# Optimization experiments

Hardware: AMD Instinct MI355X
Metric: run time of the kernel (lower is better)

## Reference

```python
import jax, jax.numpy as jnp
import numpy as np

H = 1024      # LSTM_DIM
D = 1024      # BERT_DIM
VW = 30000    # word vocab
VA = 30       # action vocab
T = 64        # transition steps
S = 512       # BERT memory length


def lstm_cell(x, h, c, Wih, Whh, bih, bhh):
    # torch.nn.LSTMCell math: gates ordered i, f, g, o
    g = x @ Wih.T + bih + h @ Whh.T + bhh
    i, f, gg, o = jnp.split(g, 4, axis=-1)
    c2 = jax.nn.sigmoid(f) * c + jax.nn.sigmoid(i) * jnp.tanh(gg)
    h2 = jax.nn.sigmoid(o) * jnp.tanh(c2)
    return h2, c2


def forward(memory, actions, words,
            term_Wih, term_Whh, term_bih, term_bhh,
            act_Wih, act_Whh, act_bih, act_bhh,
            Wq, bq, Wa1, ba1, Wa2, ba2, Ww1, bw1, Ww2, bw2,
            act_emb, word_emb):
    z = jnp.zeros((1, H), dtype=memory.dtype)

    def step(carry, xs):
        term_h, term_c, act_h, act_c, stack_h = carry
        a_t, w_t = xs
        # predict_action: concat decoder states, dot-attention over BERT memory (no softmax)
        states = jnp.concatenate([term_h, act_h, stack_h], axis=1)     # [1, 3H]
        q = states @ Wq.T + bq                                          # [1, D]
        attn = jnp.einsum('bsd,bd->bs', memory, q)                      # [1, S]
        ctx = jnp.einsum('bs,bsd->bd', attn, memory)                    # [1, D]
        final = jnp.concatenate([states, ctx], axis=1)                  # [1, 3H+D]
        act_logits = jax.nn.relu(final @ Wa1.T + ba1) @ Wa2.T + ba2     # [1, VA]
        word_logits = jax.nn.relu(final @ Ww1.T + bw1) @ Ww2.T + bw2    # [1, VW]
        # do_action: act LSTM step, then SHIFT: word embedding into term LSTM + stack push
        a_e = act_emb[a_t][None, :]
        act_h2, act_c2 = lstm_cell(a_e, act_h, act_c, act_Wih, act_Whh, act_bih, act_bhh)
        w_e = word_emb[w_t][None, :]
        term_h2, term_c2 = lstm_cell(w_e, term_h, term_c, term_Wih, term_Whh, term_bih, term_bhh)
        new_carry = (term_h2, term_c2, act_h2, act_c2, w_e)
        return new_carry, (act_logits[0], word_logits[0])

    carry0 = (z, z, z, z, z)
    _, (act_logits, word_logits) = jax.lax.scan(step, carry0, (actions, words))
    return act_logits, word_logits  # [T, VA], [T, VW]


def setup_inputs() -> dict:
    key = jax.random.key(0)
    ks = jax.random.split(key, 24)
    s = 0.02

    def n(k, shape):
        return jax.random.normal(k, shape, dtype=jnp.float32) * s

    return {
        'memory': jax.random.normal(ks[0], (1, S, D), dtype=jnp.float32),
        'actions': jax.random.randint(ks[1], (T,), 0, VA),
        'words': jax.random.randint(ks[2], (T,), 0, VW),
        'term_Wih': n(ks[3], (4 * H, H)), 'term_Whh': n(ks[4], (4 * H, H)),
        'term_bih': n(ks[5], (4 * H,)), 'term_bhh': n(ks[6], (4 * H,)),
        'act_Wih': n(ks[7], (4 * H, H)), 'act_Whh': n(ks[8], (4 * H, H)),
        'act_bih': n(ks[9], (4 * H,)), 'act_bhh': n(ks[10], (4 * H,)),
        'Wq': n(ks[11], (D, 3 * H)), 'bq': n(ks[12], (D,)),
        'Wa1': n(ks[13], (H, 3 * H + D)), 'ba1': n(ks[14], (H,)),
        'Wa2': n(ks[15], (VA, H)), 'ba2': n(ks[16], (VA,)),
        'Ww1': n(ks[17], (H, 3 * H + D)), 'bw1': n(ks[18], (H,)),
        'Ww2': n(ks[19], (VW, H)), 'bw2': n(ks[20], (VW,)),
        'act_emb': n(ks[21], (VA, H)),
        'word_emb': n(ks[22], (VW, H)),
    }


def reference(memory, actions, words,
              term_Wih, term_Whh, term_bih, term_bhh,
              act_Wih, act_Whh, act_bih, act_bhh,
              Wq, bq, Wa1, ba1, Wa2, ba2, Ww1, bw1, Ww2, bw2,
              act_emb, word_emb):
    return forward(memory, actions, words,
                   term_Wih, term_Whh, term_bih, term_bhh,
                   act_Wih, act_Whh, act_bih, act_bhh,
                   Wq, bq, Wa1, ba1, Wa2, ba2, Ww1, bw1, Ww2, bw2,
                   act_emb, word_emb)
```

## Files before the change

kernel.cpp:

```cpp
#include <hip/hip_runtime.h>

#define H 1024
#define T_STEPS 64
#define S_MEM 512
#define VA 30
#define VW 30000

typedef unsigned long long u64;
typedef __attribute__((ext_vector_type(8))) short short8;
typedef __attribute__((ext_vector_type(4))) float f32x4;

__device__ __forceinline__ float sigmf(float x) { return 1.f / (1.f + expf(-x)); }
__device__ __forceinline__ unsigned short f2bf(float f) {
  unsigned u = __float_as_uint(f);
  return (unsigned short)((u + 0x7FFFu + ((u >> 16) & 1u)) >> 16);
}
__device__ __forceinline__ short8 ldcvt8(const float* p) {
  float4 f0 = *(const float4*)p;
  float4 f1 = *(const float4*)(p + 4);
  short8 r;
  r[0] = (short)f2bf(f0.x); r[1] = (short)f2bf(f0.y);
  r[2] = (short)f2bf(f0.z); r[3] = (short)f2bf(f0.w);
  r[4] = (short)f2bf(f1.x); r[5] = (short)f2bf(f1.y);
  r[6] = (short)f2bf(f1.z); r[7] = (short)f2bf(f1.w);
  return r;
}
__device__ __forceinline__ void stage_sw(float* S, int nn, int km, float4 v) {
  int c2 = ((nn >> 2) ^ km) & 15, p = nn & 3;
  S[(km * 4 + 0) * 64 + c2 * 4 + p] = v.x;
  S[(km * 4 + 1) * 64 + c2 * 4 + p] = v.y;
  S[(km * 4 + 2) * 64 + c2 * 4 + p] = v.z;
  S[(km * 4 + 3) * 64 + c2 * 4 + p] = v.w;
}
__device__ __forceinline__ void mm_inner(const float* As, const float* Bs,
                                         int ridx, int cidx, float (&acc)[4][4]) {
  const float4* As4 = (const float4*)As;
  const float4* Bs4 = (const float4*)Bs;
  __syncthreads();
#pragma unroll 8
  for (int kk = 0; kk < 64; ++kk) {
    int sw = kk >> 2;
    float4 a4 = As4[kk * 16 + ((ridx ^ sw) & 15)];
    float4 b4 = Bs4[kk * 16 + ((cidx ^ sw) & 15)];
    float av[4] = {a4.x, a4.y, a4.z, a4.w};
    float bv[4] = {b4.x, b4.y, b4.z, b4.w};
#pragma unroll
    for (int i = 0; i < 4; ++i)
#pragma unroll
      for (int j = 0; j < 4; ++j) acc[i][j] += av[i] * bv[j];
  }
  __syncthreads();
}

__global__ __launch_bounds__(256) void k_head(
    const int* __restrict__ actions, const int* __restrict__ words,
    const float* __restrict__ act_emb, const float* __restrict__ word_emb,
    const float* __restrict__ Wih_t, const float* __restrict__ Wih_a,
    float* __restrict__ Pxg_t, float* __restrict__ Pxg_a,
    float* __restrict__ fin, u64* __restrict__ htag) {
  int x = blockIdx.x, tid = threadIdx.x, y = blockIdx.y, z = blockIdx.z;
  if (x == 64) {
    int bi = y * 2 + z;
    uint4* hq = (uint4*)(htag) + (size_t)bi * 16384;
    uint4 zz = make_uint4(0, 0, 0, 0);
    for (int i = tid; i < 16384; i += 256) hq[i] = zz;
    if (bi == 0)
      for (int i = tid; i < 3072; i += 256) fin[i] = 0.f;
    if (bi == 1) {
      for (int j = tid; j < 63 * 1024; j += 256) {
        int t = j >> 10, i2 = j & 1023;
        fin[(size_t)(t + 1) * 4096 + 2048 + i2] = word_emb[(size_t)words[t] * 1024 + i2];
      }
    }
    return;
  }
  __shared__ __align__(16) float As[4096], Bs[4096];
  const int* idxs = z ? actions : words;
  const float* emb = z ? act_emb : word_emb;
  const float* B = z ? Wih_a : Wih_t;
  float* Pp = z ? Pxg_a : Pxg_t;
  int cidx = tid & 15, ridx = tid >> 4;
  int n0 = x * 64, kbeg = y * 512;
  float acc[4][4] = {};
  for (int k0 = kbeg; k0 < kbeg + 512; k0 += 64) {
#pragma unroll
    for (int i = 0; i < 4; ++i) {
      int f = tid + i * 256, rr = f >> 4, km = f & 15;
      float4 v = *(const float4*)&emb[(size_t)idxs[rr] * 1024 + k0 + km * 4];
      stage_sw(As, rr, km, v);
    }
#pragma unroll
    for (int i = 0; i < 4; ++i) {
      int f = tid + i * 256, nn = f >> 4, km = f & 15;
      float4 v = *(const float4*)&B[(size_t)(n0 + nn) * 1024 + k0 + km * 4];
      stage_sw(Bs, nn, km, v);
    }
    mm_inner(As, Bs, ridx, cidx, acc);
  }
  int gcol = n0 + cidx * 4;
  float* P = Pp + (size_t)y * 262144;
#pragma unroll
  for (int i = 0; i < 4; ++i) {
    int row = ridx * 4 + i;
    *(float4*)&P[(size_t)row * 4096 + gcol] =
        make_float4(acc[i][0], acc[i][1], acc[i][2], acc[i][3]);
  }
}

__global__ __launch_bounds__(256, 1) void k_recur(
    const float* __restrict__ Whh_term, const float* __restrict__ Whh_act,
    const float* __restrict__ Pxg_term, const float* __restrict__ Pxg_act,
    const float* __restrict__ bih_t, const float* __restrict__ bhh_t,
    const float* __restrict__ bih_a, const float* __restrict__ bhh_a,
    float* __restrict__ fin, u64* __restrict__ htag) {
  __shared__ float hs[2][32 * 36];
  __shared__ float xgs[63 * 32];
  int b = blockIdx.x, tid = threadIdx.x;
  int lstm = b >> 7, k0 = (b & 127) * 8;
  const float* Whh = lstm ? Whh_act : Whh_term;
  const float* Pxg = lstm ? Pxg_act : Pxg_term;
  const float* bih = lstm ? bih_a : bih_t;
  const float* bhh = lstm ? bhh_a : bhh_t;
  int d = tid >> 5, p = tid & 31;

  float wreg[128];
#pragma unroll
  for (int g = 0; g < 4; ++g) {
    const float* wrow = Whh + (size_t)(g * 1024 + k0 + d) * 1024 + p * 32;
#pragma unroll
    for (int i = 0; i < 32; i += 4) {
      float4 v = *(const float4*)(wrow + i);
      wreg[g * 32 + i]     = v.x; wreg[g * 32 + i + 1] = v.y;
      wreg[g * 32 + i + 2] = v.z; wreg[g * 32 + i + 3] = v.w;
    }
  }
#pragma unroll
  for (int i = 0; i < 128; ++i) asm volatile("" : "+v"(wreg[i]));

  for (int i = tid; i < 63 * 32; i += 256) {
    int rr = i & 31, t2 = i >> 5;
    int row2 = (rr >> 3) * 1024 + k0 + (rr & 7);
    xgs[i] = Pxg[(size_t)t2 * 4096 + row2] + Pxg[262144 + (size_t)t2 * 4096 + row2] +
             bih[row2] + bhh[row2];
  }
  float c_loc = 0.f;

  for (int t = 0; t < 63; ++t) {
    float* hb = hs[t & 1];
    if (t > 0) {
      const u64* src = htag + (size_t)t * 2048 + lstm * 1024;
      u64 v0 = __hip_atomic_load(&src[tid], __ATOMIC_RELAXED, __HIP_MEMORY_SCOPE_AGENT);
      u64 v1 = __hip_atomic_load(&src[tid + 256], __ATOMIC_RELAXED, __HIP_MEMORY_SCOPE_AGENT);
      u64 v2 = __hip_atomic_load(&src[tid + 512], __ATOMIC_RELAXED, __HIP_MEMORY_SCOPE_AGENT);
      u64 v3 = __hip_atomic_load(&src[tid + 768], __ATOMIC_RELAXED, __HIP_MEMORY_SCOPE_AGENT);
      while ((unsigned)(v0 >> 32) != (unsigned)t) {
        __builtin_amdgcn_s_sleep(1);
        v0 = __hip_atomic_load(&src[tid], __ATOMIC_RELAXED, __HIP_MEMORY_SCOPE_AGENT);
      }
      while ((unsigned)(v1 >> 32) != (unsigned)t) {
        __builtin_amdgcn_s_sleep(1);
        v1 = __hip_atomic_load(&src[tid + 256], __ATOMIC_RELAXED, __HIP_MEMORY_SCOPE_AGENT);
      }
      while ((unsigned)(v2 >> 32) != (unsigned)t) {
        __builtin_amdgcn_s_sleep(1);
        v2 = __hip_atomic_load(&src[tid + 512], __ATOMIC_RELAXED, __HIP_MEMORY_SCOPE_AGENT);
      }
      while ((unsigned)(v3 >> 32) != (unsigned)t) {
        __builtin_amdgcn_s_sleep(1);
        v3 = __hip_atomic_load(&src[tid + 768], __ATOMIC_RELAXED, __HIP_MEMORY_SCOPE_AGENT);
      }
      hb[((tid) >> 5) * 36 + (tid & 31)]       = __uint_as_float((unsigned)v0);
      hb[((tid + 256) >> 5) * 36 + (tid & 31)] = __uint_as_float((unsigned)v1);
      hb[((tid + 512) >> 5) * 36 + (tid & 31)] = __uint_as_float((unsigned)v2);
      hb[((tid + 768) >> 5) * 36 + (tid & 31)] = __uint_as_float((unsigned)v3);
    } else {
#pragma unroll
      for (int j = 0; j < 4; ++j) {
        int idx = tid + j * 256;
        hb[(idx >> 5) * 36 + (idx & 31)] = 0.f;
      }
    }
    __syncthreads();

    const float* hp = hb + p * 36;
    float s0 = 0.f, s1 = 0.f, s2 = 0.f, s3 = 0.f;
#pragma unroll
    for (int i = 0; i < 32; i += 4) {
      float4 hv = *(const float4*)&hp[i];
      s0 += wreg[i] * hv.x + wreg[i + 1] * hv.y + wreg[i + 2] * hv.z + wreg[i + 3] * hv.w;
      s1 += wreg[32 + i] * hv.x + wreg[33 + i] * hv.y + wreg[34 + i] * hv.z + wreg[35 + i] * hv.w;
      s2 += wreg[64 + i] * hv.x + wreg[65 + i] * hv.y + wreg[66 + i] * hv.z + wreg[67 + i] * hv.w;
      s3 += wreg[96 + i] * hv.x + wreg[97 + i] * hv.y + wreg[98 + i] * hv.z + wreg[99 + i] * hv.w;
    }
#pragma unroll
    for (int m = 1; m <= 16; m <<= 1) {
      s0 += __shfl_xor(s0, m); s1 += __shfl_xor(s1, m);
      s2 += __shfl_xor(s2, m); s3 += __shfl_xor(s3, m);
    }
    if (p == 0) {
      float gi = s0 + xgs[t * 32 + d];
      float gf = s1 + xgs[t * 32 + 8 + d];
      float gg = s2 + xgs[t * 32 + 16 + d];
      float go = s3 + xgs[t * 32 + 24 + d];
      float c2 = sigmf(gf) * c_loc + sigmf(gi) * tanhf(gg);
      float h2 = sigmf(go) * tanhf(c2);
      c_loc = c2;
      fin[(size_t)(t + 1) * 4096 + lstm * 1024 + k0 + d] = h2;
      __hip_atomic_store(&htag[(size_t)(t + 1) * 2048 + lstm * 1024 + k0 + d],
                         (((u64)(t + 1)) << 32) | (u64)__float_as_uint(h2),
                         __ATOMIC_RELAXED, __HIP_MEMORY_SCOPE_AGENT);
    }
  }
}

__global__ __launch_bounds__(256) void k_mfma_bt(
    const float* __restrict__ A, int lda,
    const float* __restrict__ B0, const float* __restrict__ B1, int ldb,
    const float* __restrict__ bias0, const float* __restrict__ bias1,
    float* __restrict__ out0, float* __restrict__ out1, int ldc,
    int K, int relu) {
  __shared__ __align__(16) float sm[4 * 1024];
  const float* B = blockIdx.y ? B1 : B0;
  const float* bias = blockIdx.y ? bias1 : bias0;
  float* out = blockIdx.y ? out1 : out0;
  int tid = threadIdx.x;
  int w = tid >> 6, lane = tid & 63;
  int col0 = blockIdx.x * 16;
  int klen = K >> 2;
  int kbeg = w * klen;
  int kg = kbeg + (lane >> 4) * 8;
  const float* brow = B + (size_t)(col0 + (lane & 15)) * ldb + kg;
  const float* arow = A + (size_t)(lane & 15) * lda + kg;
  f32x4 acc0 = {0.f, 0.f, 0.f, 0.f}, acc1 = acc0, acc2 = acc0, acc3 = acc0;

  short8 bf = ldcvt8(brow);
  short8 a0 = ldcvt8(arow);
  short8 a1 = ldcvt8(arow + 16 * lda);
  short8 a2 = ldcvt8(arow + 32 * lda);
  short8 a3 = ldcvt8(arow + 48 * lda);
  for (int k0 = 0; k0 < klen - 32; k0 += 32) {
    short8 bf_n = ldcvt8(brow + k0 + 32);
    short8 a0n = ldcvt8(arow + k0 + 32);
    short8 a1n = ldcvt8(arow + 16 * lda + k0 + 32);
    short8 a2n = ldcvt8(arow + 32 * lda + k0 + 32);
    short8 a3n = ldcvt8(arow + 48 * lda + k0 + 32);
    acc0 = __builtin_amdgcn_mfma_f32_16x16x32_bf16(a0, bf, acc0, 0, 0, 0);
    acc1 = __builtin_amdgcn_mfma_f32_16x16x32_bf16(a1, bf, acc1, 0, 0, 0);
    acc2 = __builtin_amdgcn_mfma_f32_16x16x32_bf16(a2, bf, acc2, 0, 0, 0);
    acc3 = __builtin_amdgcn_mfma_f32_16x16x32_bf16(a3, bf, acc3, 0, 0, 0);
    bf = bf_n; a0 = a0n; a1 = a1n; a2 = a2n; a3 = a3n;
  }
  acc0 = __builtin_amdgcn_mfma_f32_16x16x32_bf16(a0, bf, acc0, 0, 0, 0);
  acc1 = __builtin_amdgcn_mfma_f32_16x16x32_bf16(a1, bf, acc1, 0, 0, 0);
  acc2 = __builtin_amdgcn_mfma_f32_16x16x32_bf16(a2, bf, acc2, 0, 0, 0);
  acc3 = __builtin_amdgcn_mfma_f32_16x16x32_bf16(a3, bf, acc3, 0, 0, 0);

  {
    int rbase = (lane >> 4) * 4, c = lane & 15;
    float* smw = sm + w * 1024;
#pragma unroll
    for (int j = 0; j < 4; ++j) {
      smw[(rbase + j) * 16 + c]      = acc0[j];
      smw[(16 + rbase + j) * 16 + c] = acc1[j];
      smw[(32 + rbase + j) * 16 + c] = acc2[j];
      smw[(48 + rbase + j) * 16 + c] = acc3[j];
    }
  }
  __syncthreads();
  {
    const float4* sm4 = (const float4*)sm;
    float4 v = sm4[tid];
    float4 v1 = sm4[256 + tid], v2 = sm4[512 + tid], v3 = sm4[768 + tid];
    v.x += v1.x + v2.x + v3.x;
    v.y += v1.y + v2.y + v3.y;
    v.z += v1.z + v2.z + v3.z;
    v.w += v1.w + v2.w + v3.w;
    int e0 = tid * 4;
    int row = e0 >> 4, cofs = e0 & 15;
    float4 b = *(const float4*)&bias[col0 + cofs];
    v.x += b.x; v.y += b.y; v.z += b.z; v.w += b.w;
    if (relu) {
      v.x = fmaxf(v.x, 0.f); v.y = fmaxf(v.y, 0.f);
      v.z = fmaxf(v.z, 0.f); v.w = fmaxf(v.w, 0.f);
    }
    *(float4*)&out[(size_t)row * ldc + col0 + cofs] = v;
  }
}

__global__ __launch_bounds__(256) void k_attn2(
    const float* __restrict__ qbuf, const float* __restrict__ mem,
    float* __restrict__ Pa) {
  __shared__ __align__(16) float As[4096], Bs[4096];
  int tid = threadIdx.x, cidx = tid & 15, ridx = tid >> 4;
  int n0 = blockIdx.x * 64, kbeg = blockIdx.y * 128;
  float acc[4][4] = {};
  for (int k0 = kbeg; k0 < kbeg + 128; k0 += 64) {
#pragma unroll
    for (int i = 0; i < 4; ++i) {
      int f = tid + i * 256, rr = f >> 4, km = f & 15;
      float4 v = *(const float4*)&qbuf[(size_t)rr * 1024 + k0 + km * 4];
      stage_sw(As, rr, km, v);
    }
#pragma unroll
    for (int i = 0; i < 4; ++i) {
      int f = tid + i * 256, nn = f >> 4, km = f & 15;
      float4 v = *(const float4*)&mem[(size_t)(n0 + nn) * 1024 + k0 + km * 4];
      stage_sw(Bs, nn, km, v);
    }
    mm_inner(As, Bs, ridx, cidx, acc);
  }
  int gcol = n0 + cidx * 4;
  float* P = Pa + (size_t)blockIdx.y * 32768;
#pragma unroll
  for (int i = 0; i < 4; ++i) {
    int row = ridx * 4 + i;
    *(float4*)&P[(size_t)row * 512 + gcol] =
        make_float4(acc[i][0], acc[i][1], acc[i][2], acc[i][3]);
  }
}

__global__ __launch_bounds__(256) void k_ctx2(
    const float* __restrict__ Pa, const float* __restrict__ mem,
    float* __restrict__ fin) {
  __shared__ __align__(16) float As[4096], Bs[4096];
  int tid = threadIdx.x, cidx = tid & 15, ridx = tid >> 4;
  int n0 = blockIdx.x * 64;
  float acc[4][4] = {};
  for (int k0 = 0; k0 < 512; k0 += 64) {
#pragma unroll
    for (int i = 0; i < 4; ++i) {
      int f = tid + i * 256, rr = f >> 4, km = f & 15;
      int col = k0 + km * 4;
      float4 v = make_float4(0.f, 0.f, 0.f, 0.f);
#pragma unroll
      for (int s = 0; s < 8; ++s) {
        float4 p = *(const float4*)&Pa[(size_t)s * 32768 + (size_t)rr * 512 + col];
        v.x += p.x; v.y += p.y; v.z += p.z; v.w += p.w;
      }
      stage_sw(As, rr, km, v);
    }
#pragma unroll
    for (int i = 0; i < 4; ++i) {
      int f = tid + i * 256, kr = f >> 4, nq = f & 15;
      float4 v = *(const float4*)&mem[(size_t)(k0 + kr) * 1024 + n0 + nq * 4];
      ((float4*)Bs)[kr * 16 + ((nq ^ (kr >> 2)) & 15)] = v;
    }
    mm_inner(As, Bs, ridx, cidx, acc);
  }
  int gcol = n0 + cidx * 4;
#pragma unroll
  for (int i = 0; i < 4; ++i) {
    int row = ridx * 4 + i;
    *(float4*)&fin[(size_t)row * 4096 + 3072 + gcol] =
        make_float4(acc[i][0], acc[i][1], acc[i][2], acc[i][3]);
  }
}

__global__ __launch_bounds__(256) void k_actlog(
    const float* __restrict__ ha, const float* __restrict__ Wa2,
    const float* __restrict__ ba2, float* __restrict__ out) {
  int t = blockIdx.x, tid = threadIdx.x;
  int v = tid >> 3, p = tid & 7;
  float sum = 0.f;
  if (v < VA) {
    const float* a  = ha + (size_t)t * 1024 + p * 128;
    const float* wr = Wa2 + (size_t)v * 1024 + p * 128;
#pragma unroll 8
    for (int i = 0; i < 128; i += 4) {
      float4 av = *(const float4*)(a + i);
      float4 wv = *(const float4*)(wr + i);
      sum += av.x * wv.x + av.y * wv.y + av.z * wv.z + av.w * wv.w;
    }
  }
  sum += __shfl_xor(sum, 1);
  sum += __shfl_xor(sum, 2);
  sum += __shfl_xor(sum, 4);
  if (p == 0 && v < VA) out[(size_t)t * VA + v] = sum + ba2[v];
}

extern "C" void kernel_launch(void* const* d_in, const int* in_sizes, int n_in,
                              void* d_out, int out_size, void* d_ws, size_t ws_size,
                              hipStream_t stream) {
  const float* memory   = (const float*)d_in[0];
  const int*   actions  = (const int*)d_in[1];
  const int*   words    = (const int*)d_in[2];
  const float* term_Wih = (const float*)d_in[3];
  const float* term_Whh = (const float*)d_in[4];
  const float* term_bih = (const float*)d_in[5];
  const float* term_bhh = (const float*)d_in[6];
  const float* act_Wih  = (const float*)d_in[7];
  const float* act_Whh  = (const float*)d_in[8];
  const float* act_bih  = (const float*)d_in[9];
  const float* act_bhh  = (const float*)d_in[10];
  const float* Wq  = (const float*)d_in[11];
  const float* bq  = (const float*)d_in[12];
  const float* Wa1 = (const float*)d_in[13];
  const float* ba1 = (const float*)d_in[14];
  const float* Wa2 = (const float*)d_in[15];
  const float* ba2 = (const float*)d_in[16];
  const float* Ww1 = (const float*)d_in[17];
  const float* bw1 = (const float*)d_in[18];
  const float* Ww2 = (const float*)d_in[19];
  const float* bw2 = (const float*)d_in[20];
  const float* act_emb  = (const float*)d_in[21];
  const float* word_emb = (const float*)d_in[22];
  float* out = (float*)d_out;

  float* w     = (float*)d_ws;
  float* fin   = w;
  u64*   htag  = (u64*)(w + 262144);
  float* Pxg_t = w + 525312;
  float* Pxg_a = w + 1049600;
  float* qbuf  = w + 525312;
  float* Pa    = w + 590848;
  float* ha    = w + 852992;
  float* hw    = w + 918528;

  k_head<<<dim3(65, 2, 2), 256, 0, stream>>>(
      actions, words, act_emb, word_emb, term_Wih, act_Wih,
      Pxg_t, Pxg_a, fin, htag);

  k_recur<<<256, 256, 0, stream>>>(term_Whh, act_Whh, Pxg_t, Pxg_a,
                                   term_bih, term_bhh, act_bih, act_bhh, fin, htag);

  k_mfma_bt<<<dim3(64, 1), 256, 0, stream>>>(
      fin, 4096, Wq, nullptr, 3072, bq, nullptr, qbuf, nullptr, 1024, 3072, 0);

  k_attn2<<<dim3(8, 8), 256, 0, stream>>>(qbuf, memory, Pa);

  k_ctx2<<<16, 256, 0, stream>>>(Pa, memory, fin);

  k_mfma_bt<<<dim3(64, 2), 256, 0, stream>>>(
      fin, 4096, Wa1, Ww1, 4096, ba1, bw1, ha, hw, 1024, 4096, 1);

  k_actlog<<<64, 256, 0, stream>>>(ha, Wa2, ba2, out);

  k_mfma_bt<<<dim3(1875, 1), 256, 0, stream>>>(
      hw, 1024, Ww2, nullptr, 1024, bw2, nullptr, out + 1920, nullptr, VW, 1024, 0);
}
```

Before: 474.6 us.

## Precompute memory Gram matrix folded into Wq, overlapped with LSTM recurrence

Because attention has no softmax, ctx equals q·(MᵀM), so the change precomputes M2=MᵀM, a transformed query weight WpT=M2·Wq and bias bq2=M2·bq. These are computed inside the recurrence kernel by extra blocks that run alongside the LSTM blocks, coordinated through an atomic counter. The separate q, attention and ctx kernels become a single split-K GEMM whose partial sums are reduced inside the Wa1/Ww1 GEMM, and the final reduction writes bf16 hw for a new word-logit MFMA kernel. The cost is the extra weight-sized work and a spin-wait in the recurrence kernel, which may compete with the latency-critical LSTM blocks. The reassociated summation order also changes floating-point rounding.

```diff
diff --git a/kernel.cpp b/kernel.cpp
--- a/kernel.cpp
+++ b/kernel.cpp
@@ -51,13 +51,25 @@
   }
   __syncthreads();
 }
+__device__ __forceinline__ void st4a(float* p, float4 v) {
+  u64 lo = ((u64)__float_as_uint(v.y) << 32) | __float_as_uint(v.x);
+  u64 hi = ((u64)__float_as_uint(v.w) << 32) | __float_as_uint(v.z);
+  __hip_atomic_store((u64*)p, lo, __ATOMIC_RELAXED, __HIP_MEMORY_SCOPE_AGENT);
+  __hip_atomic_store(((u64*)p) + 1, hi, __ATOMIC_RELAXED, __HIP_MEMORY_SCOPE_AGENT);
+}
+__device__ __forceinline__ float4 ld4a(const float* p) {
+  u64 lo = __hip_atomic_load((const u64*)p, __ATOMIC_RELAXED, __HIP_MEMORY_SCOPE_AGENT);
+  u64 hi = __hip_atomic_load(((const u64*)p) + 1, __ATOMIC_RELAXED, __HIP_MEMORY_SCOPE_AGENT);
+  return make_float4(__uint_as_float((unsigned)lo), __uint_as_float((unsigned)(lo >> 32)),
+                     __uint_as_float((unsigned)hi), __uint_as_float((unsigned)(hi >> 32)));
+}
 
 __global__ __launch_bounds__(256) void k_head(
     const int* __restrict__ actions, const int* __restrict__ words,
     const float* __restrict__ act_emb, const float* __restrict__ word_emb,
     const float* __restrict__ Wih_t, const float* __restrict__ Wih_a,
     float* __restrict__ Pxg_t, float* __restrict__ Pxg_a,
-    float* __restrict__ fin, u64* __restrict__ htag) {
+    float* __restrict__ fin, u64* __restrict__ htag, int* __restrict__ m2ctr) {
   int x = blockIdx.x, tid = threadIdx.x, y = blockIdx.y, z = blockIdx.z;
   if (x == 64) {
     int bi = y * 2 + z;
@@ -72,6 +84,7 @@
         fin[(size_t)(t + 1) * 4096 + 2048 + i2] = word_emb[(size_t)words[t] * 1024 + i2];
       }
     }
+    if (bi == 2 && tid < 8) m2ctr[tid] = 0;
     return;
   }
   __shared__ __align__(16) float As[4096], Bs[4096];
@@ -112,10 +125,93 @@
     const float* __restrict__ Pxg_term, const float* __restrict__ Pxg_act,
     const float* __restrict__ bih_t, const float* __restrict__ bhh_t,
     const float* __restrict__ bih_a, const float* __restrict__ bhh_a,
-    float* __restrict__ fin, u64* __restrict__ htag) {
+    float* __restrict__ fin, u64* __restrict__ htag,
+    const float* __restrict__ memory, const float* __restrict__ Wq,
+    const float* __restrict__ bq, float* __restrict__ M2,
+    float* __restrict__ WpT, float* __restrict__ bq2, int* __restrict__ m2ctr) {
   __shared__ float hs[2][32 * 36];
   __shared__ float xgs[63 * 32];
+  __shared__ __align__(16) float As[4096], Bs[4096];
   int b = blockIdx.x, tid = threadIdx.x;
+  int cidx = tid & 15, ridx = tid >> 4;
+
+  if (b >= 256) {
+    if (b < 512) {
+      int idx = b - 256;
+      int i0 = (idx >> 4) * 64, j0 = (idx & 15) * 64;
+      float acc[4][4] = {};
+      for (int k0 = 0; k0 < 512; k0 += 64) {
+#pragma unroll
+        for (int i = 0; i < 4; ++i) {
+          int f = tid + i * 256, kr = f >> 4, nq = f & 15;
+          float4 v = *(const float4*)&memory[(size_t)(k0 + kr) * 1024 + i0 + nq * 4];
+          ((float4*)As)[kr * 16 + ((nq ^ (kr >> 2)) & 15)] = v;
+        }
+#pragma unroll
+        for (int i = 0; i < 4; ++i) {
+          int f = tid + i * 256, kr = f >> 4, nq = f & 15;
+          float4 v = *(const float4*)&memory[(size_t)(k0 + kr) * 1024 + j0 + nq * 4];
+          ((float4*)Bs)[kr * 16 + ((nq ^ (kr >> 2)) & 15)] = v;
+        }
+        mm_inner(As, Bs, ridx, cidx, acc);
+      }
+      int gcol = j0 + cidx * 4;
+#pragma unroll
+      for (int i = 0; i < 4; ++i)
+        st4a(&M2[(size_t)(i0 + ridx * 4 + i) * 1024 + gcol],
+             make_float4(acc[i][0], acc[i][1], acc[i][2], acc[i][3]));
+      asm volatile("s_waitcnt vmcnt(0)" ::: "memory");
+      __syncthreads();
+      if (tid == 0)
+        __hip_atomic_fetch_add(&m2ctr[0], 1, __ATOMIC_RELAXED, __HIP_MEMORY_SCOPE_AGENT);
+      return;
+    }
+    if (tid == 0) {
+      while (__hip_atomic_load(&m2ctr[0], __ATOMIC_RELAXED, __HIP_MEMORY_SCOPE_AGENT) < 256)
+        __builtin_amdgcn_s_sleep(8);
+    }
+    __syncthreads();
+    if (b == 704) {
+      for (int n = tid; n < 1024; n += 256) {
+        float s = 0.f;
+        for (int d = 0; d < 1024; d += 4) {
+          float4 m = ld4a(&M2[(size_t)n * 1024 + d]);
+          float4 bv = *(const float4*)&bq[d];
+          s += m.x * bv.x + m.y * bv.y + m.z * bv.z + m.w * bv.w;
+        }
+        bq2[n] = s;
+      }
+      return;
+    }
+    int idx = b - 512;
+    for (int q = 0; q < 4; ++q) {
+      int t = idx * 4 + q;
+      int n0 = (t / 48) * 64, m0 = (t % 48) * 64;
+      float acc[4][4] = {};
+      for (int k0 = 0; k0 < 1024; k0 += 64) {
+#pragma unroll
+        for (int i = 0; i < 4; ++i) {
+          int f = tid + i * 256, rr = f >> 4, km = f & 15;
+          float4 v = ld4a(&M2[(size_t)(n0 + rr) * 1024 + k0 + km * 4]);
+          stage_sw(As, rr, km, v);
+        }
+#pragma unroll
+        for (int i = 0; i < 4; ++i) {
+          int f = tid + i * 256, kr = f >> 4, nq = f & 15;
+          float4 v = *(const float4*)&Wq[(size_t)(k0 + kr) * 3072 + m0 + nq * 4];
+          ((float4*)Bs)[kr * 16 + ((nq ^ (kr >> 2)) & 15)] = v;
+        }
+        mm_inner(As, Bs, ridx, cidx, acc);
+      }
+      int gcol = m0 + cidx * 4;
+#pragma unroll
+      for (int i = 0; i < 4; ++i)
+        *(float4*)&WpT[(size_t)(n0 + ridx * 4 + i) * 3072 + gcol] =
+            make_float4(acc[i][0], acc[i][1], acc[i][2], acc[i][3]);
+    }
+    return;
+  }
+
   int lstm = b >> 7, k0 = (b & 127) * 8;
   const float* Whh = lstm ? Whh_act : Whh_term;
   const float* Pxg = lstm ? Pxg_act : Pxg_term;
@@ -213,146 +309,118 @@
   }
 }
 
-__global__ __launch_bounds__(256) void k_mfma_bt(
+__global__ __launch_bounds__(256) void k_gemm64(
     const float* __restrict__ A, int lda,
-    const float* __restrict__ B0, const float* __restrict__ B1, int ldb,
-    const float* __restrict__ bias0, const float* __restrict__ bias1,
-    float* __restrict__ out0, float* __restrict__ out1, int ldc,
-    int K, int relu) {
-  __shared__ __align__(16) float sm[4 * 1024];
-  const float* B = blockIdx.y ? B1 : B0;
-  const float* bias = blockIdx.y ? bias1 : bias0;
-  float* out = blockIdx.y ? out1 : out0;
-  int tid = threadIdx.x;
-  int w = tid >> 6, lane = tid & 63;
-  int col0 = blockIdx.x * 16;
-  int klen = K >> 2;
-  int kbeg = w * klen;
-  int kg = kbeg + (lane >> 4) * 8;
-  const float* brow = B + (size_t)(col0 + (lane & 15)) * ldb + kg;
-  const float* arow = A + (size_t)(lane & 15) * lda + kg;
-  f32x4 acc0 = {0.f, 0.f, 0.f, 0.f}, acc1 = acc0, acc2 = acc0, acc3 = acc0;
-
-  short8 bf = ldcvt8(brow);
-  short8 a0 = ldcvt8(arow);
-  short8 a1 = ldcvt8(arow + 16 * lda);
-  short8 a2 = ldcvt8(arow + 32 * lda);
-  short8 a3 = ldcvt8(arow + 48 * lda);
-  for (int k0 = 0; k0 < klen - 32; k0 += 32) {
-    short8 bf_n = ldcvt8(brow + k0 + 32);
-    short8 a0n = ldcvt8(arow + k0 + 32);
-    short8 a1n = ldcvt8(arow + 16 * lda + k0 + 32);
-    short8 a2n = ldcvt8(arow + 32 * lda + k0 + 32);
-    short8 a3n = ldcvt8(arow + 48 * lda + k0 + 32);
-    acc0 = __builtin_amdgcn_mfma_f32_16x16x32_bf16(a0, bf, acc0, 0, 0, 0);
-    acc1 = __builtin_amdgcn_mfma_f32_16x16x32_bf16(a1, bf, acc1, 0, 0, 0);
-    acc2 = __builtin_amdgcn_mfma_f32_16x16x32_bf16(a2, bf, acc2, 0, 0, 0);
-    acc3 = __builtin_amdgcn_mfma_f32_16x16x32_bf16(a3, bf, acc3, 0, 0, 0);
-    bf = bf_n; a0 = a0n; a1 = a1n; a2 = a2n; a3 = a3n;
-  }
-  acc0 = __builtin_amdgcn_mfma_f32_16x16x32_bf16(a0, bf, acc0, 0, 0, 0);
-  acc1 = __builtin_amdgcn_mfma_f32_16x16x32_bf16(a1, bf, acc1, 0, 0, 0);
-  acc2 = __builtin_amdgcn_mfma_f32_16x16x32_bf16(a2, bf, acc2, 0, 0, 0);
-  acc3 = __builtin_amdgcn_mfma_f32_16x16x32_bf16(a3, bf, acc3, 0, 0, 0);
-
-  {
-    int rbase = (lane >> 4) * 4, c = lane & 15;
-    float* smw = sm + w * 1024;
-#pragma unroll
-    for (int j = 0; j < 4; ++j) {
-      smw[(rbase + j) * 16 + c]      = acc0[j];
-      smw[(16 + rbase + j) * 16 + c] = acc1[j];
-      smw[(32 + rbase + j) * 16 + c] = acc2[j];
-      smw[(48 + rbase + j) * 16 + c] = acc3[j];
-    }
-  }
-  __syncthreads();
-  {
-    const float4* sm4 = (const float4*)sm;
-    float4 v = sm4[tid];
-    float4 v1 = sm4[256 + tid], v2 = sm4[512 + tid], v3 = sm4[768 + tid];
-    v.x += v1.x + v2.x + v3.x;
-    v.y += v1.y + v2.y + v3.y;
-    v.z += v1.z + v2.z + v3.z;
-    v.w += v1.w + v2.w + v3.w;
-    int e0 = tid * 4;
-    int row = e0 >> 4, cofs = e0 & 15;
-    float4 b = *(const float4*)&bias[col0 + cofs];
-    v.x += b.x; v.y += b.y; v.z += b.z; v.w += b.w;
-    if (relu) {
-      v.x = fmaxf(v.x, 0.f); v.y = fmaxf(v.y, 0.f);
-      v.z = fmaxf(v.z, 0.f); v.w = fmaxf(v.w, 0.f);
-    }
-    *(float4*)&out[(size_t)row * ldc + col0 + cofs] = v;
-  }
-}
-
-__global__ __launch_bounds__(256) void k_attn2(
-    const float* __restrict__ qbuf, const float* __restrict__ mem,
-    float* __restrict__ Pa) {
-  __shared__ __align__(16) float As[4096], Bs[4096];
-  int tid = threadIdx.x, cidx = tid & 15, ridx = tid >> 4;
-  int n0 = blockIdx.x * 64, kbeg = blockIdx.y * 128;
-  float acc[4][4] = {};
-  for (int k0 = kbeg; k0 < kbeg + 128; k0 += 64) {
-#pragma unroll
-    for (int i = 0; i < 4; ++i) {
-      int f = tid + i * 256, rr = f >> 4, km = f & 15;
-      float4 v = *(const float4*)&qbuf[(size_t)rr * 1024 + k0 + km * 4];
-      stage_sw(As, rr, km, v);
-    }
-#pragma unroll
-    for (int i = 0; i < 4; ++i) {
-      int f = tid + i * 256, nn = f >> 4, km = f & 15;
-      float4 v = *(const float4*)&mem[(size_t)(n0 + nn) * 1024 + k0 + km * 4];
-      stage_sw(Bs, nn, km, v);
-    }
-    mm_inner(As, Bs, ridx, cidx, acc);
-  }
-  int gcol = n0 + cidx * 4;
-  float* P = Pa + (size_t)blockIdx.y * 32768;
-#pragma unroll
-  for (int i = 0; i < 4; ++i) {
-    int row = ridx * 4 + i;
-    *(float4*)&P[(size_t)row * 512 + gcol] =
-        make_float4(acc[i][0], acc[i][1], acc[i][2], acc[i][3]);
-  }
-}
-
-__global__ __launch_bounds__(256) void k_ctx2(
-    const float* __restrict__ Pa, const float* __restrict__ mem,
-    float* __restrict__ fin) {
+    const float* __restrict__ B, int ldb,
+    int N, int K, float* __restrict__ Ppart) {
   __shared__ __align__(16) float As[4096], Bs[4096];
   int tid = threadIdx.x, cidx = tid & 15, ridx = tid >> 4;
   int n0 = blockIdx.x * 64;
+  int klen = K / gridDim.y, kbeg = blockIdx.y * klen;
   float acc[4][4] = {};
-  for (int k0 = 0; k0 < 512; k0 += 64) {
+  for (int k0 = kbeg; k0 < kbeg + klen; k0 += 64) {
 #pragma unroll
     for (int i = 0; i < 4; ++i) {
       int f = tid + i * 256, rr = f >> 4, km = f & 15;
-      int col = k0 + km * 4;
-      float4 v = make_float4(0.f, 0.f, 0.f, 0.f);
-#pragma unroll
-      for (int s = 0; s < 8; ++s) {
-        float4 p = *(const float4*)&Pa[(size_t)s * 32768 + (size_t)rr * 512 + col];
-        v.x += p.x; v.y += p.y; v.z += p.z; v.w += p.w;
-      }
+      float4 v = *(const float4*)&A[(size_t)rr * lda + k0 + km * 4];
       stage_sw(As, rr, km, v);
     }
 #pragma unroll
     for (int i = 0; i < 4; ++i) {
-      int f = tid + i * 256, kr = f >> 4, nq = f & 15;
-      float4 v = *(const float4*)&mem[(size_t)(k0 + kr) * 1024 + n0 + nq * 4];
-      ((float4*)Bs)[kr * 16 + ((nq ^ (kr >> 2)) & 15)] = v;
+      int f = tid + i * 256, nn = f >> 4, km = f & 15;
+      float4 v = *(const float4*)&B[(size_t)(n0 + nn) * ldb + k0 + km * 4];
+      stage_sw(Bs, nn, km, v);
     }
     mm_inner(As, Bs, ridx, cidx, acc);
   }
   int gcol = n0 + cidx * 4;
+  float* P = Ppart + (size_t)blockIdx.y * 64 * N;
 #pragma unroll
   for (int i = 0; i < 4; ++i) {
     int row = ridx * 4 + i;
-    *(float4*)&fin[(size_t)row * 4096 + 3072 + gcol] =
+    *(float4*)&P[(size_t)row * N + gcol] =
         make_float4(acc[i][0], acc[i][1], acc[i][2], acc[i][3]);
+  }
+}
+
+__global__ __launch_bounds__(256) void k_gemm_dual(
+    const float* __restrict__ A0, int lda,
+    const float* __restrict__ B0, const float* __restrict__ B1, int ldb,
+    int N, int K, float* __restrict__ P0, float* __restrict__ P1,
+    const float* __restrict__ Pc2, const float* __restrict__ bq2, int kb) {
+  __shared__ __align__(16) float As[4096], Bs[4096];
+  const float* B = blockIdx.z ? B1 : B0;
+  float* Pp = blockIdx.z ? P1 : P0;
+  int tid = threadIdx.x, cidx = tid & 15, ridx = tid >> 4;
+  int n0 = blockIdx.x * 64;
+  int klen = K / gridDim.y, kbeg = blockIdx.y * klen;
+  float acc[4][4] = {};
+  for (int k0 = kbeg; k0 < kbeg + klen; k0 += 64) {
+#pragma unroll
+    for (int i = 0; i < 4; ++i) {
+      int f = tid + i * 256, rr = f >> 4, km = f & 15;
+      float4 v;
+      if (k0 >= kb) {
+        int kc = k0 - kb + km * 4;
+        float4 bb = *(const float4*)&bq2[kc];
+        v = bb;
+#pragma unroll
+        for (int s = 0; s < 8; ++s) {
+          float4 pp = *(const float4*)&Pc2[(size_t)s * 65536 + (size_t)rr * 1024 + kc];
+          v.x += pp.x; v.y += pp.y; v.z += pp.z; v.w += pp.w;
+        }
+      } else {
+        v = *(const float4*)&A0[(size_t)rr * lda + k0 + km * 4];
+      }
+      stage_sw(As, rr, km, v);
+    }
+#pragma unroll
+    for (int i = 0; i < 4; ++i) {
+      int f = tid + i * 256, nn = f >> 4, km = f & 15;
+      float4 v = *(const float4*)&B[(size_t)(n0 + nn) * ldb + k0 + km * 4];
+      stage_sw(Bs, nn, km, v);
+    }
+    mm_inner(As, Bs, ridx, cidx, acc);
+  }
+  int gcol = n0 + cidx * 4;
+  float* P = Pp + (size_t)blockIdx.y * 64 * N;
+#pragma unroll
+  for (int i = 0; i < 4; ++i) {
+    int row = ridx * 4 + i;
+    *(float4*)&P[(size_t)row * N + gcol] =
+        make_float4(acc[i][0], acc[i][1], acc[i][2], acc[i][3]);
+  }
+}
+
+__global__ __launch_bounds__(256) void k_reduce_dual(
+    const float* __restrict__ P0, const float* __restrict__ P1, int S, int N,
+    const float* __restrict__ ba0, const float* __restrict__ ba1,
+    float* __restrict__ o0, float* __restrict__ o1, int relu,
+    unsigned short* __restrict__ hwb_out) {
+  const float* P = blockIdx.y ? P1 : P0;
+  const float* bias = blockIdx.y ? ba1 : ba0;
+  float* out = blockIdx.y ? o1 : o0;
+  int q = blockIdx.x * 256 + threadIdx.x;
+  int total = 64 * N / 4;
+  if (q >= total) return;
+  int e0 = q * 4;
+  int col = e0 % N;
+  float4 v = make_float4(0, 0, 0, 0);
+  for (int s = 0; s < S; ++s) {
+    float4 p = *(const float4*)&P[(size_t)s * 64 * N + e0];
+    v.x += p.x; v.y += p.y; v.z += p.z; v.w += p.w;
+  }
+  float4 b = *(const float4*)&bias[col];
+  v.x += b.x; v.y += b.y; v.z += b.z; v.w += b.w;
+  if (relu) {
+    v.x = fmaxf(v.x, 0.f); v.y = fmaxf(v.y, 0.f);
+    v.z = fmaxf(v.z, 0.f); v.w = fmaxf(v.w, 0.f);
+  }
+  *(float4*)&out[e0] = v;
+  if (blockIdx.y == 1 && hwb_out) {
+    unsigned pk0 = (unsigned)f2bf(v.x) | ((unsigned)f2bf(v.y) << 16);
+    unsigned pk1 = (unsigned)f2bf(v.z) | ((unsigned)f2bf(v.w) << 16);
+    *(uint2*)&hwb_out[e0] = make_uint2(pk0, pk1);
   }
 }
 
@@ -376,6 +444,53 @@
   sum += __shfl_xor(sum, 2);
   sum += __shfl_xor(sum, 4);
   if (p == 0 && v < VA) out[(size_t)t * VA + v] = sum + ba2[v];
+}
+
+__global__ __launch_bounds__(256) void k_word_mfma(
+    const unsigned short* __restrict__ hwb, const float* __restrict__ Ww2,
+    const float* __restrict__ bw2, float* __restrict__ outw) {
+  int tid = threadIdx.x;
+  int wv = tid >> 6, lane = tid & 63;
+  int col = blockIdx.x * 64 + wv * 16 + (lane & 15);
+  int colr = col < VW ? col : VW - 1;
+  int kg = (lane >> 4) * 8;
+  const float* brow = Ww2 + (size_t)colr * 1024 + kg;
+  const unsigned short* arow = hwb + (size_t)(lane & 15) * 1024 + kg;
+  f32x4 acc0 = {0.f, 0.f, 0.f, 0.f}, acc1 = acc0, acc2 = acc0, acc3 = acc0;
+
+  short8 bf = ldcvt8(brow);
+  short8 a0 = *(const short8*)(arow);
+  short8 a1 = *(const short8*)(arow + 16 * 1024);
+  short8 a2 = *(const short8*)(arow + 32 * 1024);
+  short8 a3 = *(const short8*)(arow + 48 * 1024);
+  for (int k0 = 0; k0 < 992; k0 += 32) {
+    short8 bf_n = ldcvt8(brow + k0 + 32);
+    short8 a0n = *(const short8*)(arow + k0 + 32);
+    short8 a1n = *(const short8*)(arow + 16 * 1024 + k0 + 32);
+    short8 a2n = *(const short8*)(arow + 32 * 1024 + k0 + 32);
+    short8 a3n = *(const short8*)(arow + 48 * 1024 + k0 + 32);
+    acc0 = __builtin_amdgcn_mfma_f32_16x16x32_bf16(a0, bf, acc0, 0, 0, 0);
+    acc1 = __builtin_amdgcn_mfma_f32_16x16x32_bf16(a1, bf, acc1, 0, 0, 0);
+    acc2 = __builtin_amdgcn_mfma_f32_16x16x32_bf16(a2, bf, acc2, 0, 0, 0);
+    acc3 = __builtin_amdgcn_mfma_f32_16x16x32_bf16(a3, bf, acc3, 0, 0, 0);
+    bf = bf_n; a0 = a0n; a1 = a1n; a2 = a2n; a3 = a3n;
+  }
+  acc0 = __builtin_amdgcn_mfma_f32_16x16x32_bf16(a0, bf, acc0, 0, 0, 0);
+  acc1 = __builtin_amdgcn_mfma_f32_16x16x32_bf16(a1, bf, acc1, 0, 0, 0);
+  acc2 = __builtin_amdgcn_mfma_f32_16x16x32_bf16(a2, bf, acc2, 0, 0, 0);
+  acc3 = __builtin_amdgcn_mfma_f32_16x16x32_bf16(a3, bf, acc3, 0, 0, 0);
+
+  if (col < VW) {
+    float bias = bw2[col];
+    int r0 = (lane >> 4) * 4;
+#pragma unroll
+    for (int j = 0; j < 4; ++j) {
+      outw[(size_t)(r0 + j) * VW + col]      = acc0[j] + bias;
+      outw[(size_t)(16 + r0 + j) * VW + col] = acc1[j] + bias;
+      outw[(size_t)(32 + r0 + j) * VW + col] = acc2[j] + bias;
+      outw[(size_t)(48 + r0 + j) * VW + col] = acc3[j] + bias;
+    }
+  }
 }
 
 extern "C" void kernel_launch(void* const* d_in, const int* in_sizes, int n_in,
@@ -409,32 +524,35 @@
   float* w     = (float*)d_ws;
   float* fin   = w;
   u64*   htag  = (u64*)(w + 262144);
+  int*   m2ctr = (int*)(w + 524288);
   float* Pxg_t = w + 525312;
   float* Pxg_a = w + 1049600;
-  float* qbuf  = w + 525312;
-  float* Pa    = w + 590848;
-  float* ha    = w + 852992;
-  float* hw    = w + 918528;
+  float* M2    = w + 1573888;
+  float* WpT   = w + 2622464;
+  float* bq2   = w + 5768192;
+  float* Pc2   = Pxg_t;
+  float* Pha   = Pxg_a;
+  float* Phw   = M2;
+  float* ha    = w + 525312 + 0;
+  float* hw    = w + 525312 + 65536;
+  unsigned short* hwb = (unsigned short*)(w + 525312 + 131072);
 
   k_head<<<dim3(65, 2, 2), 256, 0, stream>>>(
       actions, words, act_emb, word_emb, term_Wih, act_Wih,
-      Pxg_t, Pxg_a, fin, htag);
-
-  k_recur<<<256, 256, 0, stream>>>(term_Whh, act_Whh, Pxg_t, Pxg_a,
-                                   term_bih, term_bhh, act_bih, act_bhh, fin, htag);
-
-  k_mfma_bt<<<dim3(64, 1), 256, 0, stream>>>(
-      fin, 4096, Wq, nullptr, 3072, bq, nullptr, qbuf, nullptr, 1024, 3072, 0);
-
-  k_attn2<<<dim3(8, 8), 256, 0, stream>>>(qbuf, memory, Pa);
-
-  k_ctx2<<<16, 256, 0, stream>>>(Pa, memory, fin);
-
-  k_mfma_bt<<<dim3(64, 2), 256, 0, stream>>>(
-      fin, 4096, Wa1, Ww1, 4096, ba1, bw1, ha, hw, 1024, 4096, 1);
+      Pxg_t, Pxg_a, fin, htag, m2ctr);
+
+  k_recur<<<705, 256, 0, stream>>>(
+      term_Whh, act_Whh, Pxg_t, Pxg_a,
+      term_bih, term_bhh, act_bih, act_bhh, fin, htag,
+      memory, Wq, bq, M2, WpT, bq2, m2ctr);
+
+  k_gemm64<<<dim3(16, 8), 256, 0, stream>>>(fin, 4096, WpT, 3072, 1024, 3072, Pc2);
+
+  k_gemm_dual<<<dim3(16, 8, 2), 256, 0, stream>>>(
+      fin, 4096, Wa1, Ww1, 4096, 1024, 4096, Pha, Phw, Pc2, bq2, 3072);
+  k_reduce_dual<<<dim3(64, 2), 256, 0, stream>>>(
+      Pha, Phw, 8, 1024, ba1, bw1, ha, hw, 1, hwb);
 
   k_actlog<<<64, 256, 0, stream>>>(ha, Wa2, ba2, out);
-
-  k_mfma_bt<<<dim3(1875, 1), 256, 0, stream>>>(
-      hw, 1024, Ww2, nullptr, 1024, bw2, nullptr, out + 1920, nullptr, VW, 1024, 0);
-}
+  k_word_mfma<<<469, 256, 0, stream>>>(hwb, Ww2, bw2, out + 1920);
+}
```

After: 606.5 us. +27.8%, slower.
